# Performance work log

Hardware: AMD Instinct MI355X
Metric: run time of the kernel (lower is better)

The kernel has to match this reference:

```python
import jax, jax.numpy as jnp
import numpy as np

PH, PW = 16, 16
TEMP = 1.0


def unfold(x, ph, pw):
    # x: [N, C, H, W] -> [N, C*ph*pw, L] matching F.unfold with stride == kernel
    N, C, H, W = x.shape
    x = x.reshape(N, C, H // ph, ph, W // pw, pw)
    x = x.transpose(0, 1, 3, 5, 2, 4)  # N, C, ph, pw, Hb, Wb
    return x.reshape(N, C * ph * pw, (H // ph) * (W // pw))


def grid_sample_pts(img, u_norm, v_norm):
    # img: [N, C, H, W]; u_norm, v_norm: [N, K] in [-1, 1]
    # Bilinear, zero padding, align_corners=False (PyTorch F.grid_sample default)
    N, C, H, W = img.shape
    x = ((u_norm + 1.0) * W - 1.0) * 0.5
    y = ((v_norm + 1.0) * H - 1.0) * 0.5

    def one(im, xx, yy):  # im [C,H,W]; xx,yy [K]
        x0 = jnp.floor(xx); y0 = jnp.floor(yy)
        x1 = x0 + 1.0; y1 = y0 + 1.0
        wx1 = xx - x0; wx0 = 1.0 - wx1
        wy1 = yy - y0; wy0 = 1.0 - wy1

        def g(xi, yi):
            valid = ((xi >= 0) & (xi <= W - 1) & (yi >= 0) & (yi <= H - 1)).astype(im.dtype)
            xi_c = jnp.clip(xi.astype(jnp.int32), 0, W - 1)
            yi_c = jnp.clip(yi.astype(jnp.int32), 0, H - 1)
            return im[:, yi_c, xi_c] * valid  # [C, K]

        return (g(x0, y0) * (wx0 * wy0) + g(x1, y0) * (wx1 * wy0)
                + g(x0, y1) * (wx0 * wy1) + g(x1, y1) * (wx1 * wy1))

    return jax.vmap(one)(img, x, y)  # [N, C, K]


def setup_inputs() -> dict:
    key = jax.random.key(0)
    k0, k1, k2, k3 = jax.random.split(key, 4)
    return {
        "geometry_img": jax.random.normal(k0, (4, 3, 512, 640), dtype=jnp.float32),
        "descriptors": jax.random.normal(k1, (4, 128, 512, 640), dtype=jnp.float32),
        "detector_scores": jax.random.normal(k2, (4, 1, 512, 640), dtype=jnp.float32),
        "weight_scores": jax.random.uniform(k3, (4, 1, 512, 640), dtype=jnp.float32),
    }


def reference(geometry_img, descriptors, detector_scores, weight_scores):
    N, _, H, W = geometry_img.shape
    P = PH * PW
    # pixel coordinate grids (shared across batch)
    vc, uc = jnp.meshgrid(jnp.arange(H, dtype=jnp.float32),
                          jnp.arange(W, dtype=jnp.float32), indexing="ij")
    v_p = unfold(vc[None, None], PH, PW)  # [1, P, L]
    u_p = unfold(uc[None, None], PH, PW)

    # no_gap=True: mask pixels with zero geometry
    gap = jnp.sum(geometry_img ** 2, axis=1, keepdims=True) == 0.0
    det = jnp.where(gap, jnp.float32(-20.0), detector_scores)

    det_p = unfold(det, PH, PW)  # [N, P, L]
    att = jax.nn.softmax(det_p / TEMP, axis=1)

    expected_v = jnp.sum(v_p * att, axis=1)  # [N, L]
    expected_u = jnp.sum(u_p * att, axis=1)
    keypoints_2D = jnp.stack([expected_u, expected_v], axis=2)  # [N, L, 2]

    geom_p = unfold(geometry_img, PH, PW).reshape(N, 3, P, -1)  # [N,3,P,L]
    keypoint_coords = jnp.einsum("ncpl,npl->ncl", geom_p, att)  # [N, 3, L]

    u_norm = 2.0 * expected_u / (W - 1) - 1.0
    v_norm = 2.0 * expected_v / (H - 1) - 1.0
    keypoint_descs = grid_sample_pts(descriptors, u_norm, v_norm)  # [N, C, L]
    keypoint_weights = grid_sample_pts(weight_scores, u_norm, v_norm)  # [N, 1, L]

    return keypoints_2D, keypoint_coords, keypoint_descs, keypoint_weights
```

## Files before the change

kernel.cpp:

```cpp
#include <hip/hip_runtime.h>
#include <hip/hip_bf16.h>
#include <math.h>

#define H 512
#define W 640
#define PHH 16
#define PWW 16
#define LPATCH 1280
#define WBLK 40
#define NIMG 4
#define CDESC 128

#define OFF_K2D 0
#define OFF_COORDS 10240
#define OFF_DESC  (10240 + 15360)
#define OFF_WGT   (10240 + 15360 + 655360)

__global__ __launch_bounds__(256) void kp_attn(
    const float* __restrict__ geom,
    const float* __restrict__ det,
    float* __restrict__ out)
{
    const int blk = blockIdx.x;
    const int n = blk / LPATCH;
    const int l = blk - n * LPATCH;
    const int hb = l / WBLK;
    const int wb = l - hb * WBLK;
    const int t  = threadIdx.x;
    const int pi = t >> 4;
    const int pj = t & 15;
    const int v = hb * PHH + pi;
    const int u = wb * PWW + pj;
    const size_t pix = (size_t)v * W + u;
    const size_t plane = (size_t)H * W;

    const float* gb = geom + (size_t)n * 3 * plane + pix;
    const float g0 = gb[0];
    const float g1 = gb[plane];
    const float g2 = gb[2 * plane];
    float s = det[(size_t)n * plane + pix];
    if (g0 * g0 + g1 * g1 + g2 * g2 == 0.0f) s = -20.0f;

    const int wid = t >> 6;
    __shared__ float sm[4];
    float m = s;
    #pragma unroll
    for (int off = 32; off > 0; off >>= 1) m = fmaxf(m, __shfl_xor(m, off, 64));
    if ((t & 63) == 0) sm[wid] = m;
    __syncthreads();
    m = fmaxf(fmaxf(sm[0], sm[1]), fmaxf(sm[2], sm[3]));

    const float e = __expf(s - m);
    float a0 = e;
    float a1 = e * (float)u;
    float a2 = e * (float)v;
    float a3 = e * g0;
    float a4 = e * g1;
    float a5 = e * g2;
    #pragma unroll
    for (int off = 32; off > 0; off >>= 1) {
        a0 += __shfl_xor(a0, off, 64);
        a1 += __shfl_xor(a1, off, 64);
        a2 += __shfl_xor(a2, off, 64);
        a3 += __shfl_xor(a3, off, 64);
        a4 += __shfl_xor(a4, off, 64);
        a5 += __shfl_xor(a5, off, 64);
    }
    __shared__ float ss[6][4];
    if ((t & 63) == 0) {
        ss[0][wid] = a0; ss[1][wid] = a1; ss[2][wid] = a2;
        ss[3][wid] = a3; ss[4][wid] = a4; ss[5][wid] = a5;
    }
    __syncthreads();
    if (t == 0) {
        float S  = ss[0][0] + ss[0][1] + ss[0][2] + ss[0][3];
        float Su = ss[1][0] + ss[1][1] + ss[1][2] + ss[1][3];
        float Sv = ss[2][0] + ss[2][1] + ss[2][2] + ss[2][3];
        float S0 = ss[3][0] + ss[3][1] + ss[3][2] + ss[3][3];
        float S1 = ss[4][0] + ss[4][1] + ss[4][2] + ss[4][3];
        float S2 = ss[5][0] + ss[5][1] + ss[5][2] + ss[5][3];
        const float inv = 1.0f / S;
        float* k2 = out + OFF_K2D + ((size_t)n * LPATCH + l) * 2;
        k2[0] = Su * inv;
        k2[1] = Sv * inv;
        float* oc = out + OFF_COORDS + (size_t)n * 3 * LPATCH + l;
        oc[0]          = S0 * inv;
        oc[LPATCH]     = S1 * inv;
        oc[2 * LPATCH] = S2 * inv;
    }
}

__global__ __launch_bounds__(256) void kp_sample(
    const float* __restrict__ desc,
    const float* __restrict__ wsc,
    float* __restrict__ out)
{
    int blk = blockIdx.x;
    const int lb = blk % 5;  blk /= 5;
    const int cg = blk % 65;
    const int n  = blk / 65;
    const int l  = lb * 256 + threadIdx.x;
    const size_t plane = (size_t)H * W;

    const float* k2 = out + OFF_K2D + ((size_t)n * LPATCH + l) * 2;
    const float eu = k2[0];
    const float ev = k2[1];
    const float un = 2.0f * eu / (float)(W - 1) - 1.0f;
    const float vn = 2.0f * ev / (float)(H - 1) - 1.0f;
    const float x = ((un + 1.0f) * (float)W - 1.0f) * 0.5f;
    const float y = ((vn + 1.0f) * (float)H - 1.0f) * 0.5f;
    const float x0 = floorf(x), y0 = floorf(y);
    const float x1 = x0 + 1.0f, y1 = y0 + 1.0f;
    const float wx1 = x - x0, wx0 = 1.0f - wx1;
    const float wy1 = y - y0, wy0 = 1.0f - wy1;

    const bool vx0 = (x0 >= 0.0f) && (x0 <= (float)(W - 1));
    const bool vx1 = (x1 >= 0.0f) && (x1 <= (float)(W - 1));
    const bool vy0 = (y0 >= 0.0f) && (y0 <= (float)(H - 1));
    const bool vy1 = (y1 >= 0.0f) && (y1 <= (float)(H - 1));

    const float w00 = (vx0 && vy0) ? wx0 * wy0 : 0.0f;
    const float w10 = (vx1 && vy0) ? wx1 * wy0 : 0.0f;
    const float w01 = (vx0 && vy1) ? wx0 * wy1 : 0.0f;
    const float w11 = (vx1 && vy1) ? wx1 * wy1 : 0.0f;

    int xi0 = (int)x0; xi0 = xi0 < 0 ? 0 : (xi0 > W - 1 ? W - 1 : xi0);
    int xi1 = (int)x1; xi1 = xi1 < 0 ? 0 : (xi1 > W - 1 ? W - 1 : xi1);
    int yi0 = (int)y0; yi0 = yi0 < 0 ? 0 : (yi0 > H - 1 ? H - 1 : yi0);
    int yi1 = (int)y1; yi1 = yi1 < 0 ? 0 : (yi1 > H - 1 ? H - 1 : yi1);

    const size_t o00 = (size_t)yi0 * W + xi0;
    const size_t o10 = (size_t)yi0 * W + xi1;
    const size_t o01 = (size_t)yi1 * W + xi0;
    const size_t o11 = (size_t)yi1 * W + xi1;

    if (cg < 64) {
        const float* p1 = desc + ((size_t)n * CDESC + cg) * plane;
        const float* p2 = p1 + (size_t)64 * plane;
        const float a00 = p1[o00], a10 = p1[o10], a01 = p1[o01], a11 = p1[o11];
        const float b00 = p2[o00], b10 = p2[o10], b01 = p2[o01], b11 = p2[o11];
        const float r1 = a00 * w00 + a10 * w10 + a01 * w01 + a11 * w11;
        const float r2 = b00 * w00 + b10 * w10 + b01 * w01 + b11 * w11;
        float* op = out + OFF_DESC + ((size_t)n * CDESC + cg) * LPATCH + l;
        op[0] = r1;
        op[(size_t)64 * LPATCH] = r2;
    } else {
        const float* p = wsc + (size_t)n * plane;
        const float r = p[o00] * w00 + p[o10] * w10 + p[o01] * w01 + p[o11] * w11;
        out[OFF_WGT + (size_t)n * LPATCH + l] = r;
    }
}

extern "C" void kernel_launch(void* const* d_in, const int* in_sizes, int n_in,
                              void* d_out, int out_size, void* d_ws, size_t ws_size,
                              hipStream_t stream) {
    const float* geom = (const float*)d_in[0];
    const float* desc = (const float*)d_in[1];
    const float* det  = (const float*)d_in[2];
    const float* wsc  = (const float*)d_in[3];
    float* out = (float*)d_out;

    kp_attn<<<NIMG * LPATCH, 256, 0, stream>>>(geom, det, out);
    kp_sample<<<NIMG * 65 * (LPATCH / 256), 256, 0, stream>>>(desc, wsc, out);
}
```

Measured before the change: 749.5 us.

## Map one patch per wavefront with float4 loads and precompute bilinear taps

The attention kernel now handles each 16x16 patch with one 64-lane wavefront. Each lane loads float4 vectors and does the softmax reduction with shuffles only, which removes the shared-memory round trips and block syncs. It also computes the bilinear tap weights and offsets once per keypoint and stores them in workspace. The sampling kernel reads those taps and gathers 4 channels per thread instead of 2, which cuts the number of blocks and the repeated coordinate math. A fallback kernel is used when no workspace is provided.

Measured after the change: 744.6 us. Within noise of the previous version (-0.7%).

```diff
diff --git a/kernel.cpp b/kernel.cpp
--- a/kernel.cpp
+++ b/kernel.cpp
@@ -1,110 +1,24 @@
 #include <hip/hip_runtime.h>
-#include <hip/hip_bf16.h>
 #include <math.h>
 
 #define H 512
 #define W 640
-#define PHH 16
-#define PWW 16
 #define LPATCH 1280
 #define WBLK 40
 #define NIMG 4
 #define CDESC 128
+#define PLANE ((size_t)H * W)
 
 #define OFF_K2D 0
 #define OFF_COORDS 10240
 #define OFF_DESC  (10240 + 15360)
 #define OFF_WGT   (10240 + 15360 + 655360)
 
-__global__ __launch_bounds__(256) void kp_attn(
-    const float* __restrict__ geom,
-    const float* __restrict__ det,
-    float* __restrict__ out)
-{
-    const int blk = blockIdx.x;
-    const int n = blk / LPATCH;
-    const int l = blk - n * LPATCH;
-    const int hb = l / WBLK;
-    const int wb = l - hb * WBLK;
-    const int t  = threadIdx.x;
-    const int pi = t >> 4;
-    const int pj = t & 15;
-    const int v = hb * PHH + pi;
-    const int u = wb * PWW + pj;
-    const size_t pix = (size_t)v * W + u;
-    const size_t plane = (size_t)H * W;
-
-    const float* gb = geom + (size_t)n * 3 * plane + pix;
-    const float g0 = gb[0];
-    const float g1 = gb[plane];
-    const float g2 = gb[2 * plane];
-    float s = det[(size_t)n * plane + pix];
-    if (g0 * g0 + g1 * g1 + g2 * g2 == 0.0f) s = -20.0f;
-
-    const int wid = t >> 6;
-    __shared__ float sm[4];
-    float m = s;
-    #pragma unroll
-    for (int off = 32; off > 0; off >>= 1) m = fmaxf(m, __shfl_xor(m, off, 64));
-    if ((t & 63) == 0) sm[wid] = m;
-    __syncthreads();
-    m = fmaxf(fmaxf(sm[0], sm[1]), fmaxf(sm[2], sm[3]));
-
-    const float e = __expf(s - m);
-    float a0 = e;
-    float a1 = e * (float)u;
-    float a2 = e * (float)v;
-    float a3 = e * g0;
-    float a4 = e * g1;
-    float a5 = e * g2;
-    #pragma unroll
-    for (int off = 32; off > 0; off >>= 1) {
-        a0 += __shfl_xor(a0, off, 64);
-        a1 += __shfl_xor(a1, off, 64);
-        a2 += __shfl_xor(a2, off, 64);
-        a3 += __shfl_xor(a3, off, 64);
-        a4 += __shfl_xor(a4, off, 64);
-        a5 += __shfl_xor(a5, off, 64);
-    }
-    __shared__ float ss[6][4];
-    if ((t & 63) == 0) {
-        ss[0][wid] = a0; ss[1][wid] = a1; ss[2][wid] = a2;
-        ss[3][wid] = a3; ss[4][wid] = a4; ss[5][wid] = a5;
-    }
-    __syncthreads();
-    if (t == 0) {
-        float S  = ss[0][0] + ss[0][1] + ss[0][2] + ss[0][3];
-        float Su = ss[1][0] + ss[1][1] + ss[1][2] + ss[1][3];
-        float Sv = ss[2][0] + ss[2][1] + ss[2][2] + ss[2][3];
-        float S0 = ss[3][0] + ss[3][1] + ss[3][2] + ss[3][3];
-        float S1 = ss[4][0] + ss[4][1] + ss[4][2] + ss[4][3];
-        float S2 = ss[5][0] + ss[5][1] + ss[5][2] + ss[5][3];
-        const float inv = 1.0f / S;
-        float* k2 = out + OFF_K2D + ((size_t)n * LPATCH + l) * 2;
-        k2[0] = Su * inv;
-        k2[1] = Sv * inv;
-        float* oc = out + OFF_COORDS + (size_t)n * 3 * LPATCH + l;
-        oc[0]          = S0 * inv;
-        oc[LPATCH]     = S1 * inv;
-        oc[2 * LPATCH] = S2 * inv;
-    }
-}
-
-__global__ __launch_bounds__(256) void kp_sample(
-    const float* __restrict__ desc,
-    const float* __restrict__ wsc,
-    float* __restrict__ out)
-{
-    int blk = blockIdx.x;
-    const int lb = blk % 5;  blk /= 5;
-    const int cg = blk % 65;
-    const int n  = blk / 65;
-    const int l  = lb * 256 + threadIdx.x;
-    const size_t plane = (size_t)H * W;
-
-    const float* k2 = out + OFF_K2D + ((size_t)n * LPATCH + l) * 2;
-    const float eu = k2[0];
-    const float ev = k2[1];
+__device__ __forceinline__ void make_taps(
+    float eu, float ev,
+    float& w00, float& w10, float& w01, float& w11,
+    int& o00, int& o10, int& o01, int& o11)
+{
     const float un = 2.0f * eu / (float)(W - 1) - 1.0f;
     const float vn = 2.0f * ev / (float)(H - 1) - 1.0f;
     const float x = ((un + 1.0f) * (float)W - 1.0f) * 0.5f;
@@ -119,35 +33,174 @@
     const bool vy0 = (y0 >= 0.0f) && (y0 <= (float)(H - 1));
     const bool vy1 = (y1 >= 0.0f) && (y1 <= (float)(H - 1));
 
-    const float w00 = (vx0 && vy0) ? wx0 * wy0 : 0.0f;
-    const float w10 = (vx1 && vy0) ? wx1 * wy0 : 0.0f;
-    const float w01 = (vx0 && vy1) ? wx0 * wy1 : 0.0f;
-    const float w11 = (vx1 && vy1) ? wx1 * wy1 : 0.0f;
+    w00 = (vx0 && vy0) ? wx0 * wy0 : 0.0f;
+    w10 = (vx1 && vy0) ? wx1 * wy0 : 0.0f;
+    w01 = (vx0 && vy1) ? wx0 * wy1 : 0.0f;
+    w11 = (vx1 && vy1) ? wx1 * wy1 : 0.0f;
 
     int xi0 = (int)x0; xi0 = xi0 < 0 ? 0 : (xi0 > W - 1 ? W - 1 : xi0);
     int xi1 = (int)x1; xi1 = xi1 < 0 ? 0 : (xi1 > W - 1 ? W - 1 : xi1);
     int yi0 = (int)y0; yi0 = yi0 < 0 ? 0 : (yi0 > H - 1 ? H - 1 : yi0);
     int yi1 = (int)y1; yi1 = yi1 < 0 ? 0 : (yi1 > H - 1 ? H - 1 : yi1);
 
-    const size_t o00 = (size_t)yi0 * W + xi0;
-    const size_t o10 = (size_t)yi0 * W + xi1;
-    const size_t o01 = (size_t)yi1 * W + xi0;
-    const size_t o11 = (size_t)yi1 * W + xi1;
-
-    if (cg < 64) {
-        const float* p1 = desc + ((size_t)n * CDESC + cg) * plane;
-        const float* p2 = p1 + (size_t)64 * plane;
-        const float a00 = p1[o00], a10 = p1[o10], a01 = p1[o01], a11 = p1[o11];
-        const float b00 = p2[o00], b10 = p2[o10], b01 = p2[o01], b11 = p2[o11];
-        const float r1 = a00 * w00 + a10 * w10 + a01 * w01 + a11 * w11;
-        const float r2 = b00 * w00 + b10 * w10 + b01 * w01 + b11 * w11;
+    o00 = yi0 * W + xi0;
+    o10 = yi0 * W + xi1;
+    o01 = yi1 * W + xi0;
+    o11 = yi1 * W + xi1;
+}
+
+__global__ __launch_bounds__(256) void kp_attn(
+    const float* __restrict__ geom,
+    const float* __restrict__ det,
+    float* __restrict__ out,
+    float4* __restrict__ ws)
+{
+    const int t = threadIdx.x;
+    const int wid = t >> 6;
+    const int lane = t & 63;
+    const int wave = blockIdx.x * 4 + wid;
+    const int n = wave / LPATCH;
+    const int l = wave - n * LPATCH;
+    const int hb = l / WBLK;
+    const int wb = l - hb * WBLK;
+    const int pi = lane >> 2;
+    const int pj0 = (lane & 3) << 2;
+    const int v = hb * 16 + pi;
+    const int u0 = wb * 16 + pj0;
+    const size_t pix = (size_t)v * W + u0;
+
+    const float* gb = geom + (size_t)n * 3 * PLANE + pix;
+    const float4 g0 = *(const float4*)(gb);
+    const float4 g1 = *(const float4*)(gb + PLANE);
+    const float4 g2 = *(const float4*)(gb + 2 * PLANE);
+    const float4 dv = *(const float4*)(det + (size_t)n * PLANE + pix);
+
+    float s[4]  = { dv.x, dv.y, dv.z, dv.w };
+    const float ga[4] = { g0.x, g0.y, g0.z, g0.w };
+    const float gbv[4] = { g1.x, g1.y, g1.z, g1.w };
+    const float gc[4] = { g2.x, g2.y, g2.z, g2.w };
+    #pragma unroll
+    for (int j = 0; j < 4; ++j)
+        if (ga[j] * ga[j] + gbv[j] * gbv[j] + gc[j] * gc[j] == 0.0f) s[j] = -20.0f;
+
+    float m = fmaxf(fmaxf(s[0], s[1]), fmaxf(s[2], s[3]));
+    #pragma unroll
+    for (int off = 32; off > 0; off >>= 1) m = fmaxf(m, __shfl_xor(m, off, 64));
+
+    float a0 = 0.f, a1 = 0.f, a3 = 0.f, a4 = 0.f, a5 = 0.f;
+    #pragma unroll
+    for (int j = 0; j < 4; ++j) {
+        const float e = __expf(s[j] - m);
+        a0 += e;
+        a1 += e * (float)(u0 + j);
+        a3 += e * ga[j];
+        a4 += e * gbv[j];
+        a5 += e * gc[j];
+    }
+    float a2 = (float)v * a0;
+
+    #pragma unroll
+    for (int off = 32; off > 0; off >>= 1) {
+        a0 += __shfl_xor(a0, off, 64);
+        a1 += __shfl_xor(a1, off, 64);
+        a2 += __shfl_xor(a2, off, 64);
+        a3 += __shfl_xor(a3, off, 64);
+        a4 += __shfl_xor(a4, off, 64);
+        a5 += __shfl_xor(a5, off, 64);
+    }
+
+    const float inv = 1.0f / a0;
+    const float eu = a1 * inv;
+    const float ev = a2 * inv;
+
+    float w00, w10, w01, w11;
+    int o00, o10, o01, o11;
+    make_taps(eu, ev, w00, w10, w01, w11, o00, o10, o01, o11);
+
+    if (lane == 0) {
+        float* k2 = out + OFF_K2D + (size_t)wave * 2;
+        k2[0] = eu;
+        k2[1] = ev;
+        float* oc = out + OFF_COORDS + (size_t)n * 3 * LPATCH + l;
+        oc[0]          = a3 * inv;
+        oc[LPATCH]     = a4 * inv;
+        oc[2 * LPATCH] = a5 * inv;
+        if (ws) {
+            ws[2 * wave] = make_float4(w00, w10, w01, w11);
+            ((int4*)ws)[2 * wave + 1] = make_int4(o00, o10, o01, o11);
+        }
+    }
+}
+
+__global__ __launch_bounds__(256) void kp_sample(
+    const float* __restrict__ desc,
+    const float* __restrict__ wsc,
+    const float4* __restrict__ ws,
+    float* __restrict__ out)
+{
+    int blk = blockIdx.x;
+    const int lb = blk % 5;  blk /= 5;
+    const int cg = blk % 33;
+    const int n  = blk / 33;
+    const int l  = lb * 256 + threadIdx.x;
+    const int idx = n * LPATCH + l;
+
+    const float4 wv = ws[2 * idx];
+    const int4  ov = ((const int4*)ws)[2 * idx + 1];
+
+    if (cg < 32) {
+        const float* p = desc + ((size_t)n * CDESC + cg) * PLANE;
+        float r[4];
+        #pragma unroll
+        for (int k = 0; k < 4; ++k) {
+            const float* pk = p + (size_t)k * 32 * PLANE;
+            const float t00 = pk[ov.x];
+            const float t10 = pk[ov.y];
+            const float t01 = pk[ov.z];
+            const float t11 = pk[ov.w];
+            r[k] = t00 * wv.x + t10 * wv.y + t01 * wv.z + t11 * wv.w;
+        }
         float* op = out + OFF_DESC + ((size_t)n * CDESC + cg) * LPATCH + l;
-        op[0] = r1;
-        op[(size_t)64 * LPATCH] = r2;
+        #pragma unroll
+        for (int k = 0; k < 4; ++k) op[(size_t)k * 32 * LPATCH] = r[k];
     } else {
-        const float* p = wsc + (size_t)n * plane;
-        const float r = p[o00] * w00 + p[o10] * w10 + p[o01] * w01 + p[o11] * w11;
-        out[OFF_WGT + (size_t)n * LPATCH + l] = r;
+        const float* p = wsc + (size_t)n * PLANE;
+        out[OFF_WGT + (size_t)n * LPATCH + l] =
+            p[ov.x] * wv.x + p[ov.y] * wv.y + p[ov.z] * wv.z + p[ov.w] * wv.w;
+    }
+}
+
+__global__ __launch_bounds__(256) void kp_sample_k2(
+    const float* __restrict__ desc,
+    const float* __restrict__ wsc,
+    float* __restrict__ out)
+{
+    int blk = blockIdx.x;
+    const int lb = blk % 5;  blk /= 5;
+    const int cg = blk % 33;
+    const int n  = blk / 33;
+    const int l  = lb * 256 + threadIdx.x;
+
+    const float* k2 = out + OFF_K2D + ((size_t)n * LPATCH + l) * 2;
+    float w00, w10, w01, w11;
+    int o00, o10, o01, o11;
+    make_taps(k2[0], k2[1], w00, w10, w01, w11, o00, o10, o01, o11);
+
+    if (cg < 32) {
+        const float* p = desc + ((size_t)n * CDESC + cg) * PLANE;
+        float r[4];
+        #pragma unroll
+        for (int k = 0; k < 4; ++k) {
+            const float* pk = p + (size_t)k * 32 * PLANE;
+            r[k] = pk[o00] * w00 + pk[o10] * w10 + pk[o01] * w01 + pk[o11] * w11;
+        }
+        float* op = out + OFF_DESC + ((size_t)n * CDESC + cg) * LPATCH + l;
+        #pragma unroll
+        for (int k = 0; k < 4; ++k) op[(size_t)k * 32 * LPATCH] = r[k];
+    } else {
+        const float* p = wsc + (size_t)n * PLANE;
+        out[OFF_WGT + (size_t)n * LPATCH + l] =
+            p[o00] * w00 + p[o10] * w10 + p[o01] * w01 + p[o11] * w11;
     }
 }
 
@@ -160,6 +213,14 @@
     const float* wsc  = (const float*)d_in[3];
     float* out = (float*)d_out;
 
-    kp_attn<<<NIMG * LPATCH, 256, 0, stream>>>(geom, det, out);
-    kp_sample<<<NIMG * 65 * (LPATCH / 256), 256, 0, stream>>>(desc, wsc, out);
-}
+    const size_t ws_needed = (size_t)NIMG * LPATCH * 32;
+    const bool use_ws = (d_ws != nullptr) && (ws_size >= ws_needed);
+
+    kp_attn<<<1280, 256, 0, stream>>>(geom, det, out,
+                                      use_ws ? (float4*)d_ws : nullptr);
+    if (use_ws)
+        kp_sample<<<NIMG * 33 * 5, 256, 0, stream>>>(desc, wsc,
+                                                     (const float4*)d_ws, out);
+    else
+        kp_sample_k2<<<NIMG * 33 * 5, 256, 0, stream>>>(desc, wsc, out);
+}
```
